# Kernel tuning notes

Measured on AMD Instinct MI355X. Metric: run time of the kernel, lower is better.

The kernel has to match this reference:

```python
import jax, jax.numpy as jnp
import numpy as np

T, L, C = 128, 32, 4
B, D = 32, 512


def _compute_content_matrix(T, L, C):
    # Precomputed sparse weighting tensor: for each (window start i, window end j),
    # C clip-averaging rows over the frames covered by that window.
    Wc = np.zeros((L, L, C, T), dtype=np.float32)
    for i in range(L):
        for j in range(i, L):
            window_size = j - i + 1
            window_start, num_frames = i * (T // L), window_size * (T // L)
            clip_size = max(1, num_frames // C)
            for c in range(min(C, num_frames)):
                s = window_start + c * clip_size
                Wc[i, j, c, s:s + clip_size] = 1.0 / clip_size
    return Wc


def setup_inputs() -> dict:
    key = jax.random.key(0)
    k1, k2 = jax.random.split(key)
    f = jax.random.normal(k1, (B, T, D), dtype=jnp.float32)
    moment_mask = jax.random.uniform(k2, (B, L, L), dtype=jnp.float32)
    Wc = jnp.asarray(_compute_content_matrix(T, L, C))
    return {"f": f, "moment_mask": moment_mask, "Wc": Wc}


def reference(f, moment_mask, Wc):
    # fc: [B, L, L, C, D] -- clip features per (start,end) window, masked
    fc = jnp.einsum('lmct,btd->blmcd', Wc, f) * moment_mask[:, :, :, None, None]
    # fm: [B, L, L, D] -- mean over clips
    fm = jnp.mean(fc, axis=3)
    # fb: [B, L, D] -- boundary features = non-overlapping avg pool of size T//L
    b, t, d = f.shape
    l = Wc.shape[0]
    fb = f.reshape(b, l, t // l, d).mean(axis=2)
    return (fc, fm, fb)
```

## Files before the change

kernel.cpp:

```cpp
#include <hip/hip_runtime.h>

#define TT 128
#define LL 32
#define CC 4
#define BB 32
#define DD 512
#define D4 (DD / 4)

typedef float fx4 __attribute__((ext_vector_type(4)));

__device__ __forceinline__ void nt_store(fx4 v, const fx4* p) {
    __builtin_nontemporal_store(v, (fx4*)p);
}

__device__ __forceinline__ fx4 diff_scale(fx4 a, fx4 b, float s) {
    return (a - b) * s;
}

__global__ __launch_bounds__(64) void prefix_kernel(const fx4* __restrict__ f4,
                                                    fx4* __restrict__ P4) {
    int idx = blockIdx.x * 64 + threadIdx.x;
    int b = idx >> 7;
    int d4 = idx & (D4 - 1);
    const fx4* fp = f4 + (size_t)b * TT * D4 + d4;
    fx4* Pp = P4 + (size_t)b * (TT + 1) * D4 + d4;
    fx4 acc = (fx4)0.f;
    Pp[0] = acc;
#pragma unroll 16
    for (int t = 0; t < TT; ++t) {
        acc += fp[(size_t)t * D4];
        Pp[(size_t)(t + 1) * D4] = acc;
    }
}

__global__ __launch_bounds__(128) void fcfm_kernel(const fx4* __restrict__ P4,
                                                   const float* __restrict__ mask,
                                                   fx4* __restrict__ fc4,
                                                   fx4* __restrict__ fm4,
                                                   fx4* __restrict__ fb4) {
    int h = blockIdx.x;
    int blk = ((h & 7) << 12) | (h >> 3);
    int j = blk & (LL - 1);
    int i = (blk >> 5) & (LL - 1);
    int b = blk >> 10;
    int tid = threadIdx.x;
    fx4* fc_out = fc4 + (size_t)blk * CC * D4 + tid;
    fx4* fm_out = fm4 + (size_t)blk * D4 + tid;

    if (j < i) {
        fx4 z = (fx4)0.f;
        nt_store(z, fc_out);
        nt_store(z, fc_out + D4);
        nt_store(z, fc_out + 2 * D4);
        nt_store(z, fc_out + 3 * D4);
        nt_store(z, fm_out);
        return;
    }

    int ws = j - i + 1;
    float sc = mask[blk] / (float)ws;
    float sm = 0.25f * sc;
    const fx4* Pb = P4 + (size_t)b * (TT + 1) * D4 + tid;
    int s0 = 4 * i;

    fx4 p0 = Pb[(size_t)(s0) * D4];
    fx4 p1 = Pb[(size_t)(s0 + ws) * D4];
    fx4 p2 = Pb[(size_t)(s0 + 2 * ws) * D4];
    fx4 p3 = Pb[(size_t)(s0 + 3 * ws) * D4];
    fx4 p4 = Pb[(size_t)(s0 + 4 * ws) * D4];

    nt_store(diff_scale(p1, p0, sc), fc_out);
    nt_store(diff_scale(p2, p1, sc), fc_out + D4);
    nt_store(diff_scale(p3, p2, sc), fc_out + 2 * D4);
    nt_store(diff_scale(p4, p3, sc), fc_out + 3 * D4);
    nt_store(diff_scale(p4, p0, sm), fm_out);

    if (j == i) {
        nt_store(diff_scale(p4, p0, 0.25f),
                 fb4 + ((size_t)b * LL + i) * D4 + tid);
    }
}

__global__ __launch_bounds__(256) void fcfm_direct(const float* __restrict__ f,
                                                   const float* __restrict__ mask,
                                                   float* __restrict__ fc,
                                                   float* __restrict__ fm) {
    int blk = blockIdx.x;
    int j = blk & (LL - 1);
    int i = (blk >> 5) & (LL - 1);
    int b = blk >> 10;
    int tid = threadIdx.x;
    float* fc_out = fc + (size_t)blk * CC * DD;
    float* fm_out = fm + (size_t)blk * DD;

    if (j < i) {
        fx4 z = (fx4)0.f;
        fx4* fcv = (fx4*)fc_out;
#pragma unroll
        for (int k = 0; k < 2; ++k) fcv[tid + k * 256] = z;
        fx4* fmv = (fx4*)fm_out;
        if (tid < DD / 4) fmv[tid] = z;
        return;
    }

    int ws = j - i + 1;
    float sc = mask[blk] / (float)ws;
    const float* fbase = f + (size_t)b * TT * DD;

#pragma unroll
    for (int r = 0; r < 2; ++r) {
        int dd = tid + r * 256;
        float tot = 0.f;
#pragma unroll
        for (int c = 0; c < CC; ++c) {
            float s = 0.f;
            int t0 = 4 * i + c * ws;
            for (int t = 0; t < ws; ++t) s += fbase[(size_t)(t0 + t) * DD + dd];
            fc_out[c * DD + dd] = s * sc;
            tot += s;
        }
        fm_out[dd] = tot * sc * 0.25f;
    }
}

__global__ __launch_bounds__(256) void fb_direct(const float* __restrict__ f,
                                                 float* __restrict__ fb) {
    int idx = blockIdx.x * 256 + threadIdx.x;
    int d = idx & (DD - 1);
    int l = (idx >> 9) & (LL - 1);
    int b = idx >> 14;
    const float* fp = f + (size_t)b * TT * DD + d;
    int t0 = 4 * l;
    fb[idx] = (fp[(size_t)t0 * DD] + fp[(size_t)(t0 + 1) * DD] +
               fp[(size_t)(t0 + 2) * DD] + fp[(size_t)(t0 + 3) * DD]) * 0.25f;
}

extern "C" void kernel_launch(void* const* d_in, const int* in_sizes, int n_in,
                              void* d_out, int out_size, void* d_ws, size_t ws_size,
                              hipStream_t stream) {
    const float* f    = (const float*)d_in[0];
    const float* mask = (const float*)d_in[1];

    float* out = (float*)d_out;
    const size_t fc_elems = (size_t)BB * LL * LL * CC * DD;
    const size_t fm_elems = (size_t)BB * LL * LL * DD;
    float* fc = out;
    float* fm = out + fc_elems;
    float* fb = out + fc_elems + fm_elems;

    const size_t P_bytes = (size_t)BB * (TT + 1) * DD * sizeof(float);

    if (ws_size >= P_bytes) {
        float* P = (float*)d_ws;
        prefix_kernel<<<(BB * D4) / 64, 64, 0, stream>>>((const fx4*)f,
                                                         (fx4*)P);
        fcfm_kernel<<<BB * LL * LL, 128, 0, stream>>>((const fx4*)P, mask,
                                                      (fx4*)fc, (fx4*)fm,
                                                      (fx4*)fb);
    } else {
        fcfm_direct<<<BB * LL * LL, 256, 0, stream>>>(f, mask, fc, fm);
        fb_direct<<<(BB * LL * DD) / 256, 256, 0, stream>>>(f, fb);
    }
}
```

Measured before the change: 356.4 us.

## Replace per-window block kernel with flat grid-stride kernel over all outputs

Replaces the one-block-per-(b,i,j) fc/fm kernel with a single grid-stride kernel of 2048 blocks of 256 threads. It walks the fc, fm and fb output arrays linearly, and each element reads two prefix-sum rows and writes one contiguous vector. The aim is to keep stores in address order and spread work evenly, in place of many small 128-thread blocks. In exchange, each fc element reloads prefix rows that the old code shared across the four clips, so prefix-buffer reads roughly double. It also swaps the division for an approximate reciprocal.

```diff
diff --git a/kernel.cpp b/kernel.cpp
--- a/kernel.cpp
+++ b/kernel.cpp
@@ -11,10 +11,6 @@
 
 __device__ __forceinline__ void nt_store(fx4 v, const fx4* p) {
     __builtin_nontemporal_store(v, (fx4*)p);
-}
-
-__device__ __forceinline__ fx4 diff_scale(fx4 a, fx4 b, float s) {
-    return (a - b) * s;
 }
 
 __global__ __launch_bounds__(64) void prefix_kernel(const fx4* __restrict__ f4,
@@ -33,51 +29,66 @@
     }
 }
 
-__global__ __launch_bounds__(128) void fcfm_kernel(const fx4* __restrict__ P4,
-                                                   const float* __restrict__ mask,
-                                                   fx4* __restrict__ fc4,
-                                                   fx4* __restrict__ fm4,
-                                                   fx4* __restrict__ fb4) {
-    int h = blockIdx.x;
-    int blk = ((h & 7) << 12) | (h >> 3);
-    int j = blk & (LL - 1);
-    int i = (blk >> 5) & (LL - 1);
-    int b = blk >> 10;
-    int tid = threadIdx.x;
-    fx4* fc_out = fc4 + (size_t)blk * CC * D4 + tid;
-    fx4* fm_out = fm4 + (size_t)blk * D4 + tid;
+__global__ __launch_bounds__(256) void fused_flat(const fx4* __restrict__ P4,
+                                                  const float* __restrict__ mask,
+                                                  fx4* __restrict__ out) {
+    const size_t FC4 = (size_t)BB * LL * LL * CC * D4;
+    const size_t FM4 = (size_t)BB * LL * LL * D4;
+    const size_t FB4 = (size_t)BB * LL * D4;
+    const size_t stride = (size_t)gridDim.x * 256;
+    const size_t t0 = (size_t)blockIdx.x * 256 + threadIdx.x;
 
-    if (j < i) {
-        fx4 z = (fx4)0.f;
-        nt_store(z, fc_out);
-        nt_store(z, fc_out + D4);
-        nt_store(z, fc_out + 2 * D4);
-        nt_store(z, fc_out + 3 * D4);
-        nt_store(z, fm_out);
-        return;
+    fx4* fc = out;
+    fx4* fm = out + FC4;
+    fx4* fb = out + FC4 + FM4;
+
+    for (size_t idx = t0; idx < FC4; idx += stride) {
+        int d4 = (int)idx & (D4 - 1);
+        int row = (int)(idx >> 7);
+        int c = row & (CC - 1);
+        int blk = row >> 2;
+        int j = blk & (LL - 1);
+        int i = (blk >> 5) & (LL - 1);
+        int b = blk >> 10;
+        fx4 v = (fx4)0.f;
+        if (j >= i) {
+            int ws = j - i + 1;
+            const fx4* Pl = P4 + (size_t)(b * (TT + 1) + 4 * i + c * ws) * D4 + d4;
+            fx4 lo = Pl[0];
+            fx4 hi = Pl[(size_t)ws * D4];
+            float sc = mask[blk] * __builtin_amdgcn_rcpf((float)ws);
+            v = (hi - lo) * sc;
+        }
+        nt_store(v, fc + idx);
     }
 
-    int ws = j - i + 1;
-    float sc = mask[blk] / (float)ws;
-    float sm = 0.25f * sc;
-    const fx4* Pb = P4 + (size_t)b * (TT + 1) * D4 + tid;
-    int s0 = 4 * i;
+    for (size_t idx = t0; idx < FM4; idx += stride) {
+        int d4 = (int)idx & (D4 - 1);
+        int blk = (int)(idx >> 7);
+        int j = blk & (LL - 1);
+        int i = (blk >> 5) & (LL - 1);
+        int b = blk >> 10;
+        fx4 v = (fx4)0.f;
+        if (j >= i) {
+            int ws = j - i + 1;
+            const fx4* Pb = P4 + (size_t)(b * (TT + 1)) * D4 + d4;
+            fx4 lo = Pb[(size_t)(4 * i) * D4];
+            fx4 hi = Pb[(size_t)(4 * i + 4 * ws) * D4];
+            float sc = 0.25f * mask[blk] * __builtin_amdgcn_rcpf((float)ws);
+            v = (hi - lo) * sc;
+        }
+        nt_store(v, fm + idx);
+    }
 
-    fx4 p0 = Pb[(size_t)(s0) * D4];
-    fx4 p1 = Pb[(size_t)(s0 + ws) * D4];
-    fx4 p2 = Pb[(size_t)(s0 + 2 * ws) * D4];
-    fx4 p3 = Pb[(size_t)(s0 + 3 * ws) * D4];
-    fx4 p4 = Pb[(size_t)(s0 + 4 * ws) * D4];
-
-    nt_store(diff_scale(p1, p0, sc), fc_out);
-    nt_store(diff_scale(p2, p1, sc), fc_out + D4);
-    nt_store(diff_scale(p3, p2, sc), fc_out + 2 * D4);
-    nt_store(diff_scale(p4, p3, sc), fc_out + 3 * D4);
-    nt_store(diff_scale(p4, p0, sm), fm_out);
-
-    if (j == i) {
-        nt_store(diff_scale(p4, p0, 0.25f),
-                 fb4 + ((size_t)b * LL + i) * D4 + tid);
+    for (size_t idx = t0; idx < FB4; idx += stride) {
+        int d4 = (int)idx & (D4 - 1);
+        int bl = (int)(idx >> 7);
+        int l = bl & (LL - 1);
+        int b = bl >> 5;
+        const fx4* Pb = P4 + (size_t)(b * (TT + 1)) * D4 + d4;
+        fx4 lo = Pb[(size_t)(4 * l) * D4];
+        fx4 hi = Pb[(size_t)(4 * l + 4) * D4];
+        nt_store((hi - lo) * 0.25f, fb + idx);
     }
 }
 
@@ -154,9 +165,7 @@
         float* P = (float*)d_ws;
         prefix_kernel<<<(BB * D4) / 64, 64, 0, stream>>>((const fx4*)f,
                                                          (fx4*)P);
-        fcfm_kernel<<<BB * LL * LL, 128, 0, stream>>>((const fx4*)P, mask,
-                                                      (fx4*)fc, (fx4*)fm,
-                                                      (fx4*)fb);
+        fused_flat<<<2048, 256, 0, stream>>>((const fx4*)P, mask, (fx4*)out);
     } else {
         fcfm_direct<<<BB * LL * LL, 256, 0, stream>>>(f, mask, fc, fm);
         fb_direct<<<(BB * LL * DD) / 256, 256, 0, stream>>>(f, fb);
```

Result: slower. 380.9 us (+6.9%).
